# Kernel tuning notes

Hardware: AMD Instinct MI355X
Metric: run time of the kernel (lower is better)

Reference implementation:

```python
import jax, jax.numpy as jnp
import numpy as np

B, S, D, H, L, FF = 1, 2048, 512, 8, 4, 2048
DH = D // H


def _sincos(n, d):
    theta = 1.0 / (10000.0 ** (np.arange(0, d, 2, dtype=np.float64) / d))
    ang = np.arange(n, dtype=np.float64)[:, None] * theta[None, :]
    sin = np.repeat(np.sin(ang), 2, axis=-1).astype(np.float32)
    cos = np.repeat(np.cos(ang), 2, axis=-1).astype(np.float32)
    return jnp.asarray(sin), jnp.asarray(cos)  # [n, d]


def _rot(x):
    # rotate pairs: (x1, x2) -> (-x2, x1), interleaved
    x1, x2 = x[..., 0::2], x[..., 1::2]
    return jnp.stack([-x2, x1], axis=-1).reshape(x.shape)


def _theta_shift(x, sin, cos):
    return x * cos + _rot(x) * sin


def _decay_mask(n, h):
    # RetNet per-head decay gammas: 1 - exp(linspace(log(1/32), log(1/512), h))
    gammas = 1.0 - np.exp(np.linspace(np.log(1.0 / 32.0), np.log(1.0 / 512.0), h))
    dist = np.arange(n)[:, None] - np.arange(n)[None, :]
    m = np.where(dist >= 0, gammas[:, None, None] ** np.maximum(dist, 0), 0.0)
    return jnp.asarray(m, dtype=jnp.float32)  # [h, n, n]


def _ln(x, w, b, eps=1e-5):
    mu = x.mean(-1, keepdims=True)
    var = ((x - mu) ** 2).mean(-1, keepdims=True)
    return (x - mu) * jax.lax.rsqrt(var + eps) * w + b


def setup_inputs() -> dict:
    key = jax.random.key(0)
    ks = jax.random.split(key, 12)
    sc = 0.02
    nrm = lambda k, shp: jax.random.normal(k, shp, jnp.float32) * sc
    return {
        "x": jax.random.normal(ks[0], (B, S, D), jnp.float32),
        "pos_emb": nrm(ks[1], (5000, D)),
        "Wq": nrm(ks[2], (L, D, D)), "bq": jnp.zeros((L, D), jnp.float32),
        "Wk": nrm(ks[3], (L, D, D)), "bk": jnp.zeros((L, D), jnp.float32),
        "Wv": nrm(ks[4], (L, D, D)), "bv": jnp.zeros((L, D), jnp.float32),
        "Wg": nrm(ks[5], (L, D, D)), "bg": jnp.zeros((L, D), jnp.float32),
        "Wo": nrm(ks[6], (L, D, D)), "bo": jnp.zeros((L, D), jnp.float32),
        "ln1w": jnp.ones((L, D), jnp.float32), "ln1b": jnp.zeros((L, D), jnp.float32),
        "ln2w": jnp.ones((L, D), jnp.float32), "ln2b": jnp.zeros((L, D), jnp.float32),
        "W1": nrm(ks[7], (L, D, FF)), "b1": jnp.zeros((L, FF), jnp.float32),
        "W2": nrm(ks[8], (L, FF, D)), "b2": jnp.zeros((L, D), jnp.float32),
        "Wout": nrm(ks[9], (D, 1)), "bout": jnp.zeros((1,), jnp.float32),
    }


def reference(x, pos_emb, Wq, bq, Wk, bk, Wv, bv, Wg, bg, Wo, bo,
              ln1w, ln1b, ln2w, ln2b, W1, b1, W2, b2, Wout, bout):
    b, s, d = x.shape
    # faithful to source: pos_emb[:x.shape[0]] (requires B==1 to broadcast)
    x = x + pos_emb[: x.shape[0]]
    sin, cos = _sincos(s, DH)
    dmask = _decay_mask(s, H)  # [h, s, s]
    inv_scale = 1.0 / jnp.sqrt(jnp.float32(DH))

    def heads(t):  # [b,s,d] -> [b,h,s,dh]
        return t.reshape(b, s, H, DH).transpose(0, 2, 1, 3)

    for l in range(L):
        # --- multi-scale retention block (pre-LN) ---
        y = _ln(x, ln1w[l], ln1b[l])
        q = heads(y @ Wq[l] + bq[l])
        k = heads(y @ Wk[l] + bk[l])
        v = heads(y @ Wv[l] + bv[l])
        q = _theta_shift(q, sin, cos) * inv_scale
        k = _theta_shift(k, sin, cos)
        sim = jnp.einsum("bhnd,bhmd->bhnm", q, k) * dmask  # decay-masked QK^T
        ret = jnp.einsum("bhnm,bhmd->bhnd", sim, v)
        # per-head group norm (no affine)
        mu = ret.mean(-1, keepdims=True)
        var = ((ret - mu) ** 2).mean(-1, keepdims=True)
        ret = (ret - mu) * jax.lax.rsqrt(var + 1e-6)
        ret = ret.transpose(0, 2, 1, 3).reshape(b, s, d)
        g = jax.nn.silu(y @ Wg[l] + bg[l])
        x = x + (g * ret) @ Wo[l] + bo[l]
        # --- FFN block (pre-LN, swish) ---
        z = _ln(x, ln2w[l], ln2b[l])
        x = x + jax.nn.silu(z @ W1[l] + b1[l]) @ W2[l] + b2[l]

    return jax.nn.sigmoid(x @ Wout + bout)  # [b, s, 1]
```

## Files before the change

kernel.cpp:

```cpp
#include <hip/hip_runtime.h>
#include <math.h>
#include <stdint.h>

#define SEQ 2048
#define DMODEL 512
#define NH 8
#define DHEAD 64
#define NL 4
#define DFF 2048

typedef __attribute__((ext_vector_type(8))) short short8;
typedef __attribute__((ext_vector_type(4))) float f32x4;

__device__ __forceinline__ short f2bf(float f) {
  unsigned u = __float_as_uint(f);
  u += 0x7fffu + ((u >> 16) & 1u);
  return (short)(u >> 16);
}
__device__ __forceinline__ float silu_f(float x) { return x / (1.f + __expf(-x)); }

__device__ __forceinline__ void cp16(const void* g, void* l) {
  __builtin_amdgcn_global_load_lds(
      (const __attribute__((address_space(1))) unsigned*)(unsigned long long)(uintptr_t)g,
      (__attribute__((address_space(3))) unsigned*)(unsigned)(uintptr_t)l, 16, 0, 0);
}

struct TP { const float* src; short* dst; int rows, cols, base; };
struct TPs { TP t[7]; };
__global__ __launch_bounds__(256) void k_prep(TPs ts) {
  int bid = blockIdx.x;
  int di = 6;
  while (di > 0 && bid < ts.t[di].base) --di;
  TP d = ts.t[di];
  int local = bid - d.base;
  int tx = d.cols >> 5, ty = d.rows >> 5;
  int tpz = tx * ty;
  int z = local / tpz, rem = local - z * tpz;
  int bx = (rem % tx) * 32, by = (rem / tx) * 32;
  const float* src = d.src + (size_t)z * d.rows * d.cols;
  short* dst = d.dst + (size_t)z * d.rows * d.cols;
  __shared__ float tile[32][33];
  int txi = threadIdx.x & 31, tyi = threadIdx.x >> 5;
#pragma unroll
  for (int k = 0; k < 4; ++k)
    tile[tyi + k * 8][txi] = src[(size_t)(by + tyi + k * 8) * d.cols + bx + txi];
  __syncthreads();
#pragma unroll
  for (int k = 0; k < 4; ++k)
    dst[(size_t)(bx + tyi + k * 8) * d.rows + by + txi] = f2bf(tile[txi][tyi + k * 8]);
}

__global__ void k_init(const float* __restrict__ xi, const float* __restrict__ pos, float* __restrict__ xo,
                       float* __restrict__ sn, float* __restrict__ cs) {
  if (blockIdx.x < 1024) {
    int i = blockIdx.x * 256 + threadIdx.x;
    float4 a = ((const float4*)xi)[i];
    float4 p = ((const float4*)pos)[i & 127];
    a.x += p.x; a.y += p.y; a.z += p.z; a.w += p.w;
    ((float4*)xo)[i] = a;
  } else {
    int g = (blockIdx.x - 1024) * 256 + threadIdx.x;
    int s = g >> 5, p = g & 31;
    double inv = pow(10000.0, -(double)p / 32.0);
    double a = (double)s * inv;
    float sv = (float)sin(a), cv = (float)cos(a);
    sn[s * DHEAD + 2 * p] = sv; sn[s * DHEAD + 2 * p + 1] = sv;
    cs[s * DHEAD + 2 * p] = cv; cs[s * DHEAD + 2 * p + 1] = cv;
  }
}

__global__ __launch_bounds__(256) void k_ln(const float* __restrict__ x, const float* __restrict__ parts, int np,
                                            const float* __restrict__ w, const float* __restrict__ b,
                                            short* __restrict__ o, float eps, float* __restrict__ xout) {
  int wid = threadIdx.x >> 6, lane = threadIdx.x & 63;
  int row = blockIdx.x * 4 + wid;
  size_t base = (size_t)row * DMODEL + lane * 8;
  float4 v0 = *(const float4*)(x + base);
  float4 v1 = *(const float4*)(x + base + 4);
  for (int p = 0; p < np; ++p) {
    const float* pp = parts + (size_t)p * SEQ * DMODEL;
    float4 a0 = *(const float4*)(pp + base);
    float4 a1 = *(const float4*)(pp + base + 4);
    v0.x += a0.x; v0.y += a0.y; v0.z += a0.z; v0.w += a0.w;
    v1.x += a1.x; v1.y += a1.y; v1.z += a1.z; v1.w += a1.w;
  }
  if (xout) {
    *(float4*)(xout + base) = v0;
    *(float4*)(xout + base + 4) = v1;
  }
  float sm = v0.x + v0.y + v0.z + v0.w + v1.x + v1.y + v1.z + v1.w;
  float sq = v0.x * v0.x + v0.y * v0.y + v0.z * v0.z + v0.w * v0.w +
             v1.x * v1.x + v1.y * v1.y + v1.z * v1.z + v1.w * v1.w;
#pragma unroll
  for (int m = 1; m < 64; m <<= 1) { sm += __shfl_xor(sm, m); sq += __shfl_xor(sq, m); }
  float mu = sm * (1.f / 512.f);
  float rstd = rsqrtf(sq * (1.f / 512.f) - mu * mu + eps);
  const float* wr = w + lane * 8; const float* br = b + lane * 8;
  float vals[8] = {v0.x, v0.y, v0.z, v0.w, v1.x, v1.y, v1.z, v1.w};
  short t[8] __attribute__((aligned(16)));
#pragma unroll
  for (int i = 0; i < 8; ++i) t[i] = f2bf((vals[i] - mu) * rstd * wr[i] + br[i]);
  *(int4*)(o + (size_t)row * DMODEL + lane * 8) = *(int4*)t;
}

struct GB { const short* Bt; const float* bias; void* out; int mode; };
struct GP {
  const short* A;
  const float* sn; const float* cs;
  GB b[4];
  int M, N, K, kspl;
};

template <int BNT>
__global__ __launch_bounds__(256) void k_gemm(GP ga) {
  constexpr int NB = BNT / 32;
  constexpr int BRND = BNT / 32;
  const int z = blockIdx.z;
  GB gb; int k0, klen;
  if (ga.kspl > 0) { gb = ga.b[0]; k0 = z * ga.kspl; klen = ga.kspl; }
  else { gb = ga.b[z]; k0 = 0; klen = ga.K; }
  const int K = ga.K, N = ga.N, M = ga.M;
  const int n0 = blockIdx.x * BNT, m0 = blockIdx.y * 64;
  const int tid = threadIdx.x;
  const int w = tid >> 6, lane = tid & 63, l16 = lane & 15, quad = lane >> 4;
  const int wm = (w & 1) * 32, wn = (w >> 1) * (BNT / 2);
  const int nIter = klen >> 6;

  __shared__ __align__(16) short As[2][4096];
  __shared__ __align__(16) short Bs[2][BNT * 64];

  const short* Ab = ga.A + (size_t)m0 * K + k0;
  const short* Bb = gb.Bt + (size_t)n0 * K + k0;
  const int rsub = lane >> 3, cch = (lane & 7) ^ rsub;

  auto stage = [&](int buf, int it) {
#pragma unroll
    for (int c = 0; c < 2; ++c) {
      int seg = w + 4 * c;
      cp16(Ab + (size_t)(seg * 8 + rsub) * K + (it << 6) + cch * 8, &As[buf][seg * 512]);
    }
#pragma unroll
    for (int c = 0; c < BRND; ++c) {
      int seg = w + 4 * c;
      cp16(Bb + (size_t)(seg * 8 + rsub) * K + (it << 6) + cch * 8, &Bs[buf][seg * 512]);
    }
  };

  f32x4 acc[2][NB];
#pragma unroll
  for (int a = 0; a < 2; ++a)
#pragma unroll
    for (int b = 0; b < NB; ++b) acc[a][b] = {0.f, 0.f, 0.f, 0.f};

  stage(0, 0);
  for (int it = 0; it < nIter; ++it) {
    __syncthreads();
    if (it + 1 < nIter) stage((it + 1) & 1, it + 1);
    const short* as = As[it & 1];
    const short* bs = Bs[it & 1];
#pragma unroll
    for (int kki = 0; kki < 2; ++kki) {
      int ch = ((quad + 4 * kki) ^ (l16 & 7)) * 8;
      short8 af[2], bfv[NB];
#pragma unroll
      for (int a = 0; a < 2; ++a) af[a] = *(const short8*)&as[(wm + a * 16 + l16) * 64 + ch];
#pragma unroll
      for (int b = 0; b < NB; ++b) bfv[b] = *(const short8*)&bs[(wn + b * 16 + l16) * 64 + ch];
#pragma unroll
      for (int a = 0; a < 2; ++a)
#pragma unroll
        for (int b = 0; b < NB; ++b)
          acc[a][b] = __builtin_amdgcn_mfma_f32_16x16x32_bf16(af[a], bfv[b], acc[a][b], 0, 0, 0);
    }
  }

  const int mode = gb.mode;
#pragma unroll
  for (int a = 0; a < 2; ++a) {
#pragma unroll
    for (int b = 0; b < NB; ++b) {
      int row0 = m0 + wm + a * 16 + quad * 4;
      int col = n0 + wn + b * 16 + l16;
      float bi = (mode == 2 && z > 0) ? 0.f : gb.bias[col];
      float vals[4];
#pragma unroll
      for (int r = 0; r < 4; ++r) vals[r] = acc[a][b][r] + bi;
      if (mode == 5 || mode == 6) {
        float sc = (mode == 5) ? 0.125f : 1.f;
        int d = col & 63;
#pragma unroll
        for (int r = 0; r < 4; ++r) {
          int s = row0 + r;
          float vv = vals[r];
          float p = __shfl_xor(vv, 1);
          float rot = (col & 1) ? p : -p;
          float o = (vv * ga.cs[s * 64 + d] + rot * ga.sn[s * 64 + d]) * sc;
          ((short*)gb.out)[(size_t)s * DMODEL + col] = f2bf(o);
        }
      } else if (mode == 4) {
        short t4[4] __attribute__((aligned(8)));
#pragma unroll
        for (int r = 0; r < 4; ++r) t4[r] = f2bf(vals[r]);
        *(uint2*)&((short*)gb.out)[(size_t)col * M + row0] = *(const uint2*)t4;
      } else if (mode == 0) {
#pragma unroll
        for (int r = 0; r < 4; ++r) ((float*)gb.out)[(size_t)(row0 + r) * N + col] = vals[r];
      } else if (mode == 1) {
#pragma unroll
        for (int r = 0; r < 4; ++r) ((short*)gb.out)[(size_t)(row0 + r) * N + col] = f2bf(silu_f(vals[r]));
      } else {
        float* po = (float*)gb.out + (size_t)z * M * N;
#pragma unroll
        for (int r = 0; r < 4; ++r) po[(size_t)(row0 + r) * N + col] = vals[r];
      }
    }
  }
}

__global__ __launch_bounds__(256) void k_attn(const short* __restrict__ qb, const short* __restrict__ kb,
                                              const short* __restrict__ vtb, float* __restrict__ r0,
                                              float* __restrict__ r1) {
  int x = blockIdx.x, hd = blockIdx.y, jc = blockIdx.z;
  int ib = jc ? (31 - x) : x;
  int t = threadIdx.x;
  int w = t >> 6, lane = t & 63, l16 = lane & 15, quad = lane >> 4;
  __shared__ __align__(16) short smem[4 * 64 * 72];
  short* qs = smem;
  short* kt = smem + 4608;
  short* vt = smem + 9216;
  short* p  = smem + 13824;

  double stepd = (log(1.0 / 512.0) - log(1.0 / 32.0)) / 7.0;
  double gam = 1.0 - exp(log(1.0 / 32.0) + hd * stepd);
  float l2g = (float)(log(gam) * 1.4426950408889634);

  for (int c = t; c < 512; c += 256) {
    int r = c >> 3, d8 = (c & 7) * 8;
    *(short8*)&qs[r * 72 + d8] = *(const short8*)&qb[(size_t)(ib * 64 + r) * DMODEL + hd * DHEAD + d8];
  }
  f32x4 oacc[4];
#pragma unroll
  for (int b = 0; b < 4; ++b) oacc[b] = {0.f, 0.f, 0.f, 0.f};

  for (int jb = jc; jb <= ib; jb += 2) {
    __syncthreads();
    for (int c = t; c < 512; c += 256) {
      int r = c >> 3, d8 = (c & 7) * 8;
      *(short8*)&kt[r * 72 + d8] = *(const short8*)&kb[(size_t)(jb * 64 + r) * DMODEL + hd * DHEAD + d8];
      *(short8*)&vt[r * 72 + d8] = *(const short8*)&vtb[(size_t)(hd * DHEAD + r) * SEQ + jb * 64 + d8];
    }
    __syncthreads();
    f32x4 sacc[4];
#pragma unroll
    for (int b = 0; b < 4; ++b) sacc[b] = {0.f, 0.f, 0.f, 0.f};
#pragma unroll
    for (int kk = 0; kk < 64; kk += 32) {
      short8 af = *(const short8*)&qs[(w * 16 + l16) * 72 + kk + quad * 8];
#pragma unroll
      for (int b = 0; b < 4; ++b) {
        short8 bf_ = *(const short8*)&kt[(b * 16 + l16) * 72 + kk + quad * 8];
        sacc[b] = __builtin_amdgcn_mfma_f32_16x16x32_bf16(af, bf_, sacc[b], 0, 0, 0);
      }
    }
    int dtile = (ib - jb) * 64;
#pragma unroll
    for (int b = 0; b < 4; ++b) {
#pragma unroll
      for (int r = 0; r < 4; ++r) {
        int iloc = w * 16 + quad * 4 + r;
        int jloc = b * 16 + l16;
        int df = dtile + iloc - jloc;
        float dec = (df < 0) ? 0.f : exp2f(l2g * (float)df);
        p[iloc * 72 + jloc] = f2bf(sacc[b][r] * dec);
      }
    }
    __syncthreads();
#pragma unroll
    for (int kk = 0; kk < 64; kk += 32) {
      short8 af = *(const short8*)&vt[(w * 16 + l16) * 72 + kk + quad * 8];
#pragma unroll
      for (int b = 0; b < 4; ++b) {
        short8 bf_ = *(const short8*)&p[(b * 16 + l16) * 72 + kk + quad * 8];
        oacc[b] = __builtin_amdgcn_mfma_f32_16x16x32_bf16(af, bf_, oacc[b], 0, 0, 0);
      }
    }
  }
  __syncthreads();
  float* obuf = (float*)smem;
#pragma unroll
  for (int b = 0; b < 4; ++b) {
#pragma unroll
    for (int r = 0; r < 4; ++r) {
      int d = w * 16 + quad * 4 + r;
      int i = b * 16 + l16;
      obuf[i * 68 + d] = oacc[b][r];
    }
  }
  __syncthreads();
  float* rp = jc ? r1 : r0;
  for (int c = t; c < 1024; c += 256) {
    int r = c >> 4, d4 = (c & 15) * 4;
    *(float4*)&rp[(size_t)(ib * 64 + r) * DMODEL + hd * DHEAD + d4] = *(const float4*)&obuf[r * 68 + d4];
  }
}

__global__ __launch_bounds__(256) void k_retgate(const float* __restrict__ r0, const float* __restrict__ r1,
                                                 const float* __restrict__ g, short* __restrict__ o) {
  int wid = threadIdx.x >> 6, lane = threadIdx.x & 63;
  int row = blockIdx.x * 4 + wid;
  int s = row >> 3, hd = row & 7;
  size_t base = (size_t)s * DMODEL + hd * DHEAD + lane;
  float v = r0[base] + r1[base];
  float sm = v, sq = v * v;
#pragma unroll
  for (int m = 1; m < 64; m <<= 1) { sm += __shfl_xor(sm, m); sq += __shfl_xor(sq, m); }
  float mu = sm * (1.f / 64.f);
  float var = sq * (1.f / 64.f) - mu * mu;
  float rn = (v - mu) * rsqrtf(var + 1e-6f);
  o[base] = f2bf(silu_f(g[base]) * rn);
}

__global__ __launch_bounds__(256) void k_final(const float* __restrict__ x, const float* __restrict__ parts, int np,
                                               const float* __restrict__ w, const float* __restrict__ bo,
                                               float* __restrict__ o) {
  int wid = threadIdx.x >> 6, lane = threadIdx.x & 63;
  int row = blockIdx.x * 4 + wid;
  size_t base = (size_t)row * DMODEL + lane * 8;
  float4 a0 = *(const float4*)(x + base), a1 = *(const float4*)(x + base + 4);
  for (int p = 0; p < np; ++p) {
    const float* pp = parts + (size_t)p * SEQ * DMODEL;
    float4 b0 = *(const float4*)(pp + base);
    float4 b1 = *(const float4*)(pp + base + 4);
    a0.x += b0.x; a0.y += b0.y; a0.z += b0.z; a0.w += b0.w;
    a1.x += b1.x; a1.y += b1.y; a1.z += b1.z; a1.w += b1.w;
  }
  float4 w0 = *(const float4*)(w + lane * 8), w1 = *(const float4*)(w + lane * 8 + 4);
  float sm = a0.x * w0.x + a0.y * w0.y + a0.z * w0.z + a0.w * w0.w +
             a1.x * w1.x + a1.y * w1.y + a1.z * w1.z + a1.w * w1.w;
#pragma unroll
  for (int m = 1; m < 64; m <<= 1) sm += __shfl_xor(sm, m);
  if (lane == 0) o[row] = 1.f / (1.f + __expf(-(sm + bo[0])));
}

extern "C" void kernel_launch(void* const* d_in, const int* in_sizes, int n_in,
                              void* d_out, int out_size, void* d_ws, size_t ws_size,
                              hipStream_t stream) {
  const float* x_in = (const float*)d_in[0];
  const float* pos = (const float*)d_in[1];
  const float* Wq = (const float*)d_in[2];  const float* bq = (const float*)d_in[3];
  const float* Wk = (const float*)d_in[4];  const float* bk = (const float*)d_in[5];
  const float* Wv = (const float*)d_in[6];  const float* bv = (const float*)d_in[7];
  const float* Wg = (const float*)d_in[8];  const float* bg = (const float*)d_in[9];
  const float* Wo = (const float*)d_in[10]; const float* bo = (const float*)d_in[11];
  const float* ln1w = (const float*)d_in[12]; const float* ln1b = (const float*)d_in[13];
  const float* ln2w = (const float*)d_in[14]; const float* ln2b = (const float*)d_in[15];
  const float* W1 = (const float*)d_in[16]; const float* b1 = (const float*)d_in[17];
  const float* W2 = (const float*)d_in[18]; const float* b2 = (const float*)d_in[19];
  const float* Wout = (const float*)d_in[20]; const float* bout = (const float*)d_in[21];
  float* out = (float*)d_out;

  char* ws = (char*)d_ws;
  size_t off = 0;
  auto alloc = [&](size_t bytes) -> void* {
    void* p = ws + off;
    off += (bytes + 255) & ~(size_t)255;
    return p;
  };
  const size_t DD = (size_t)DMODEL * DMODEL;
  const size_t SD = (size_t)SEQ * DMODEL;
  short* wqt = (short*)alloc((size_t)NL * DD * 2);
  short* wkt = (short*)alloc((size_t)NL * DD * 2);
  short* wvt = (short*)alloc((size_t)NL * DD * 2);
  short* wgt = (short*)alloc((size_t)NL * DD * 2);
  short* wot = (short*)alloc((size_t)NL * DD * 2);
  short* w1t = (short*)alloc((size_t)NL * DMODEL * DFF * 2);
  short* w2t = (short*)alloc((size_t)NL * DMODEL * DFF * 2);
  float* xb = (float*)alloc(SD * 4);
  short* ybf = (short*)alloc(SD * 2);
  float* graw = (float*)alloc(SD * 4);
  short* qb = (short*)alloc(SD * 2);
  short* kb = (short*)alloc(SD * 2);
  short* vtb = (short*)alloc(SD * 2);
  float* ret0 = (float*)alloc(SD * 4);
  float* ret1 = (float*)alloc(SD * 4);
  short* grb = (short*)alloc(SD * 2);
  short* zbf = (short*)alloc(SD * 2);
  short* hbf = (short*)alloc((size_t)SEQ * DFF * 2);
  float* sint = (float*)alloc((size_t)SEQ * DHEAD * 4);
  float* cost = (float*)alloc((size_t)SEQ * DHEAD * 4);
  float* wpart = (float*)alloc(2 * SD * 4);
  float* fpart = (float*)alloc(4 * SD * 4);

  TPs tp;
  tp.t[0] = TP{Wq, wqt, DMODEL, DMODEL, 0};
  tp.t[1] = TP{Wk, wkt, DMODEL, DMODEL, 1024};
  tp.t[2] = TP{Wv, wvt, DMODEL, DMODEL, 2048};
  tp.t[3] = TP{Wg, wgt, DMODEL, DMODEL, 3072};
  tp.t[4] = TP{Wo, wot, DMODEL, DMODEL, 4096};
  tp.t[5] = TP{W1, w1t, DMODEL, DFF, 5120};
  tp.t[6] = TP{W2, w2t, DFF, DMODEL, 9216};
  k_prep<<<13312, 256, 0, stream>>>(tp);
  k_init<<<1280, 256, 0, stream>>>(x_in, pos, xb, sint, cost);

  for (int l = 0; l < NL; ++l) {
    k_ln<<<SEQ / 4, 256, 0, stream>>>(xb, fpart, l == 0 ? 0 : 4,
                                      ln1w + l * DMODEL, ln1b + l * DMODEL, ybf, 1e-5f,
                                      l == 0 ? nullptr : xb);

    GP gq{};
    gq.A = ybf; gq.sn = sint; gq.cs = cost;
    gq.b[0] = GB{wqt + l * DD, bq + l * DMODEL, qb, 5};
    gq.b[1] = GB{wkt + l * DD, bk + l * DMODEL, kb, 6};
    gq.b[2] = GB{wvt + l * DD, bv + l * DMODEL, vtb, 4};
    gq.b[3] = GB{wgt + l * DD, bg + l * DMODEL, graw, 0};
    gq.M = SEQ; gq.N = DMODEL; gq.K = DMODEL; gq.kspl = 0;
    k_gemm<64><<<dim3(DMODEL / 64, SEQ / 64, 4), 256, 0, stream>>>(gq);

    k_attn<<<dim3(32, NH, 2), 256, 0, stream>>>(qb, kb, vtb, ret0, ret1);
    k_retgate<<<SEQ * NH / 4, 256, 0, stream>>>(ret0, ret1, graw, grb);

    GP gw{};
    gw.A = grb;
    gw.b[0] = GB{wot + l * DD, bo + l * DMODEL, wpart, 2};
    gw.M = SEQ; gw.N = DMODEL; gw.K = DMODEL; gw.kspl = 256;
    k_gemm<64><<<dim3(DMODEL / 64, SEQ / 64, 2), 256, 0, stream>>>(gw);

    k_ln<<<SEQ / 4, 256, 0, stream>>>(xb, wpart, 2,
                                      ln2w + l * DMODEL, ln2b + l * DMODEL, zbf, 1e-5f, xb);

    GP g1{};
    g1.A = zbf;
    g1.b[0] = GB{w1t + (size_t)l * DMODEL * DFF, b1 + l * DFF, hbf, 1};
    g1.M = SEQ; g1.N = DFF; g1.K = DMODEL; g1.kspl = 0;
    k_gemm<64><<<dim3(DFF / 64, SEQ / 64, 1), 256, 0, stream>>>(g1);

    GP g2{};
    g2.A = hbf;
    g2.b[0] = GB{w2t + (size_t)l * DMODEL * DFF, b2 + l * DMODEL, fpart, 2};
    g2.M = SEQ; g2.N = DMODEL; g2.K = DFF; g2.kspl = 512;
    k_gemm<64><<<dim3(DMODEL / 64, SEQ / 64, 4), 256, 0, stream>>>(g2);
  }
  k_final<<<SEQ / 4, 256, 0, stream>>>(xb, fpart, 4, Wout, bout, out);
}
```

Before: 521.0 us.

## Enlarge GEMM tiles to 128 rows and fuse QKVG weights into one wide GEMM

The QKVG projection weights are packed into one contiguous [4*512, 512] transposed buffer per layer. A single wide GEMM now covers all four, picking each output's epilogue by column block instead of by grid z. The GEMM kernel tile grows from 64 to 128 rows, and to 128 columns for the QKVG and FFN1 GEMMs, to raise data reuse per block and cut loads from global memory. The trade-off is fewer blocks per launch and more registers per thread, which may leave CUs underused.

```diff
diff --git a/kernel.cpp b/kernel.cpp
--- a/kernel.cpp
+++ b/kernel.cpp
@@ -25,7 +25,7 @@
       (__attribute__((address_space(3))) unsigned*)(unsigned)(uintptr_t)l, 16, 0, 0);
 }
 
-struct TP { const float* src; short* dst; int rows, cols, base; };
+struct TP { const float* src; short* dst; int rows, cols, base, lstride; };
 struct TPs { TP t[7]; };
 __global__ __launch_bounds__(256) void k_prep(TPs ts) {
   int bid = blockIdx.x;
@@ -38,7 +38,7 @@
   int z = local / tpz, rem = local - z * tpz;
   int bx = (rem % tx) * 32, by = (rem / tx) * 32;
   const float* src = d.src + (size_t)z * d.rows * d.cols;
-  short* dst = d.dst + (size_t)z * d.rows * d.cols;
+  short* dst = d.dst + (size_t)z * d.lstride;
   __shared__ float tile[32][33];
   int txi = threadIdx.x & 31, tyi = threadIdx.x >> 5;
 #pragma unroll
@@ -108,26 +108,28 @@
   const short* A;
   const float* sn; const float* cs;
   GB b[4];
-  int M, N, K, kspl;
+  int M, N, K, kspl, wide;
 };
 
-template <int BNT>
+template <int BN>
 __global__ __launch_bounds__(256) void k_gemm(GP ga) {
-  constexpr int NB = BNT / 32;
-  constexpr int BRND = BNT / 32;
+  constexpr int NBW = BN / 32;
+  constexpr int ARND = 4;
+  constexpr int BRND = BN / 32;
   const int z = blockIdx.z;
   GB gb; int k0, klen;
   if (ga.kspl > 0) { gb = ga.b[0]; k0 = z * ga.kspl; klen = ga.kspl; }
-  else { gb = ga.b[z]; k0 = 0; klen = ga.K; }
+  else { gb = ga.b[0]; k0 = 0; klen = ga.K; }
   const int K = ga.K, N = ga.N, M = ga.M;
-  const int n0 = blockIdx.x * BNT, m0 = blockIdx.y * 64;
+  const int n0 = blockIdx.x * BN, m0 = blockIdx.y * 128;
+  if (ga.wide) gb = ga.b[n0 >> 9];
   const int tid = threadIdx.x;
   const int w = tid >> 6, lane = tid & 63, l16 = lane & 15, quad = lane >> 4;
-  const int wm = (w & 1) * 32, wn = (w >> 1) * (BNT / 2);
+  const int wm = (w & 1) * 64, wn = (w >> 1) * (BN / 2);
   const int nIter = klen >> 6;
 
-  __shared__ __align__(16) short As[2][4096];
-  __shared__ __align__(16) short Bs[2][BNT * 64];
+  __shared__ __align__(16) short As[2][8192];
+  __shared__ __align__(16) short Bs[2][BN * 64];
 
   const short* Ab = ga.A + (size_t)m0 * K + k0;
   const short* Bb = gb.Bt + (size_t)n0 * K + k0;
@@ -135,7 +137,7 @@
 
   auto stage = [&](int buf, int it) {
 #pragma unroll
-    for (int c = 0; c < 2; ++c) {
+    for (int c = 0; c < ARND; ++c) {
       int seg = w + 4 * c;
       cp16(Ab + (size_t)(seg * 8 + rsub) * K + (it << 6) + cch * 8, &As[buf][seg * 512]);
     }
@@ -146,11 +148,11 @@
     }
   };
 
-  f32x4 acc[2][NB];
-#pragma unroll
-  for (int a = 0; a < 2; ++a)
-#pragma unroll
-    for (int b = 0; b < NB; ++b) acc[a][b] = {0.f, 0.f, 0.f, 0.f};
+  f32x4 acc[4][NBW];
+#pragma unroll
+  for (int a = 0; a < 4; ++a)
+#pragma unroll
+    for (int b = 0; b < NBW; ++b) acc[a][b] = {0.f, 0.f, 0.f, 0.f};
 
   stage(0, 0);
   for (int it = 0; it < nIter; ++it) {
@@ -161,57 +163,58 @@
 #pragma unroll
     for (int kki = 0; kki < 2; ++kki) {
       int ch = ((quad + 4 * kki) ^ (l16 & 7)) * 8;
-      short8 af[2], bfv[NB];
-#pragma unroll
-      for (int a = 0; a < 2; ++a) af[a] = *(const short8*)&as[(wm + a * 16 + l16) * 64 + ch];
-#pragma unroll
-      for (int b = 0; b < NB; ++b) bfv[b] = *(const short8*)&bs[(wn + b * 16 + l16) * 64 + ch];
-#pragma unroll
-      for (int a = 0; a < 2; ++a)
-#pragma unroll
-        for (int b = 0; b < NB; ++b)
+      short8 af[4], bfv[NBW];
+#pragma unroll
+      for (int a = 0; a < 4; ++a) af[a] = *(const short8*)&as[(wm + a * 16 + l16) * 64 + ch];
+#pragma unroll
+      for (int b = 0; b < NBW; ++b) bfv[b] = *(const short8*)&bs[(wn + b * 16 + l16) * 64 + ch];
+#pragma unroll
+      for (int a = 0; a < 4; ++a)
+#pragma unroll
+        for (int b = 0; b < NBW; ++b)
           acc[a][b] = __builtin_amdgcn_mfma_f32_16x16x32_bf16(af[a], bfv[b], acc[a][b], 0, 0, 0);
     }
   }
 
   const int mode = gb.mode;
 #pragma unroll
-  for (int a = 0; a < 2; ++a) {
-#pragma unroll
-    for (int b = 0; b < NB; ++b) {
+  for (int a = 0; a < 4; ++a) {
+#pragma unroll
+    for (int b = 0; b < NBW; ++b) {
       int row0 = m0 + wm + a * 16 + quad * 4;
       int col = n0 + wn + b * 16 + l16;
-      float bi = (mode == 2 && z > 0) ? 0.f : gb.bias[col];
+      int colO = ga.wide ? (col & 511) : col;
+      float bi = (mode == 2 && z > 0) ? 0.f : gb.bias[colO];
       float vals[4];
 #pragma unroll
       for (int r = 0; r < 4; ++r) vals[r] = acc[a][b][r] + bi;
       if (mode == 5 || mode == 6) {
         float sc = (mode == 5) ? 0.125f : 1.f;
-        int d = col & 63;
+        int d = colO & 63;
 #pragma unroll
         for (int r = 0; r < 4; ++r) {
           int s = row0 + r;
           float vv = vals[r];
           float p = __shfl_xor(vv, 1);
-          float rot = (col & 1) ? p : -p;
+          float rot = (colO & 1) ? p : -p;
           float o = (vv * ga.cs[s * 64 + d] + rot * ga.sn[s * 64 + d]) * sc;
-          ((short*)gb.out)[(size_t)s * DMODEL + col] = f2bf(o);
+          ((short*)gb.out)[(size_t)s * DMODEL + colO] = f2bf(o);
         }
       } else if (mode == 4) {
         short t4[4] __attribute__((aligned(8)));
 #pragma unroll
         for (int r = 0; r < 4; ++r) t4[r] = f2bf(vals[r]);
-        *(uint2*)&((short*)gb.out)[(size_t)col * M + row0] = *(const uint2*)t4;
+        *(uint2*)&((short*)gb.out)[(size_t)colO * M + row0] = *(const uint2*)t4;
       } else if (mode == 0) {
 #pragma unroll
-        for (int r = 0; r < 4; ++r) ((float*)gb.out)[(size_t)(row0 + r) * N + col] = vals[r];
+        for (int r = 0; r < 4; ++r) ((float*)gb.out)[(size_t)(row0 + r) * DMODEL + colO] = vals[r];
       } else if (mode == 1) {
 #pragma unroll
         for (int r = 0; r < 4; ++r) ((short*)gb.out)[(size_t)(row0 + r) * N + col] = f2bf(silu_f(vals[r]));
       } else {
-        float* po = (float*)gb.out + (size_t)z * M * N;
-#pragma unroll
-        for (int r = 0; r < 4; ++r) po[(size_t)(row0 + r) * N + col] = vals[r];
+        float* po = (float*)gb.out + (size_t)z * M * DMODEL;
+#pragma unroll
+        for (int r = 0; r < 4; ++r) po[(size_t)(row0 + r) * DMODEL + colO] = vals[r];
       }
     }
   }
@@ -368,10 +371,7 @@
   };
   const size_t DD = (size_t)DMODEL * DMODEL;
   const size_t SD = (size_t)SEQ * DMODEL;
-  short* wqt = (short*)alloc((size_t)NL * DD * 2);
-  short* wkt = (short*)alloc((size_t)NL * DD * 2);
-  short* wvt = (short*)alloc((size_t)NL * DD * 2);
-  short* wgt = (short*)alloc((size_t)NL * DD * 2);
+  short* wqkvg = (short*)alloc((size_t)NL * 4 * DD * 2);
   short* wot = (short*)alloc((size_t)NL * DD * 2);
   short* w1t = (short*)alloc((size_t)NL * DMODEL * DFF * 2);
   short* w2t = (short*)alloc((size_t)NL * DMODEL * DFF * 2);
@@ -392,13 +392,13 @@
   float* fpart = (float*)alloc(4 * SD * 4);
 
   TPs tp;
-  tp.t[0] = TP{Wq, wqt, DMODEL, DMODEL, 0};
-  tp.t[1] = TP{Wk, wkt, DMODEL, DMODEL, 1024};
-  tp.t[2] = TP{Wv, wvt, DMODEL, DMODEL, 2048};
-  tp.t[3] = TP{Wg, wgt, DMODEL, DMODEL, 3072};
-  tp.t[4] = TP{Wo, wot, DMODEL, DMODEL, 4096};
-  tp.t[5] = TP{W1, w1t, DMODEL, DFF, 5120};
-  tp.t[6] = TP{W2, w2t, DFF, DMODEL, 9216};
+  tp.t[0] = TP{Wq, wqkvg + 0 * DD, DMODEL, DMODEL, 0, (int)(4 * DD)};
+  tp.t[1] = TP{Wk, wqkvg + 1 * DD, DMODEL, DMODEL, 1024, (int)(4 * DD)};
+  tp.t[2] = TP{Wv, wqkvg + 2 * DD, DMODEL, DMODEL, 2048, (int)(4 * DD)};
+  tp.t[3] = TP{Wg, wqkvg + 3 * DD, DMODEL, DMODEL, 3072, (int)(4 * DD)};
+  tp.t[4] = TP{Wo, wot, DMODEL, DMODEL, 4096, (int)DD};
+  tp.t[5] = TP{W1, w1t, DMODEL, DFF, 5120, DMODEL * DFF};
+  tp.t[6] = TP{W2, w2t, DFF, DMODEL, 9216, DMODEL * DFF};
   k_prep<<<13312, 256, 0, stream>>>(tp);
   k_init<<<1280, 256, 0, stream>>>(x_in, pos, xb, sint, cost);
 
@@ -409,12 +409,12 @@
 
     GP gq{};
     gq.A = ybf; gq.sn = sint; gq.cs = cost;
-    gq.b[0] = GB{wqt + l * DD, bq + l * DMODEL, qb, 5};
-    gq.b[1] = GB{wkt + l * DD, bk + l * DMODEL, kb, 6};
-    gq.b[2] = GB{wvt + l * DD, bv + l * DMODEL, vtb, 4};
-    gq.b[3] = GB{wgt + l * DD, bg + l * DMODEL, graw, 0};
-    gq.M = SEQ; gq.N = DMODEL; gq.K = DMODEL; gq.kspl = 0;
-    k_gemm<64><<<dim3(DMODEL / 64, SEQ / 64, 4), 256, 0, stream>>>(gq);
+    gq.b[0] = GB{wqkvg + (size_t)l * 4 * DD, bq + l * DMODEL, qb, 5};
+    gq.b[1] = GB{wqkvg + (size_t)l * 4 * DD, bk + l * DMODEL, kb, 6};
+    gq.b[2] = GB{wqkvg + (size_t)l * 4 * DD, bv + l * DMODEL, vtb, 4};
+    gq.b[3] = GB{wqkvg + (size_t)l * 4 * DD, bg + l * DMODEL, graw, 0};
+    gq.M = SEQ; gq.N = 4 * DMODEL; gq.K = DMODEL; gq.kspl = 0; gq.wide = 1;
+    k_gemm<128><<<dim3(16, SEQ / 128, 1), 256, 0, stream>>>(gq);
 
     k_attn<<<dim3(32, NH, 2), 256, 0, stream>>>(qb, kb, vtb, ret0, ret1);
     k_retgate<<<SEQ * NH / 4, 256, 0, stream>>>(ret0, ret1, graw, grb);
@@ -422,8 +422,8 @@
     GP gw{};
     gw.A = grb;
     gw.b[0] = GB{wot + l * DD, bo + l * DMODEL, wpart, 2};
-    gw.M = SEQ; gw.N = DMODEL; gw.K = DMODEL; gw.kspl = 256;
-    k_gemm<64><<<dim3(DMODEL / 64, SEQ / 64, 2), 256, 0, stream>>>(gw);
+    gw.M = SEQ; gw.N = DMODEL; gw.K = DMODEL; gw.kspl = 256; gw.wide = 0;
+    k_gemm<64><<<dim3(DMODEL / 64, SEQ / 128, 2), 256, 0, stream>>>(gw);
 
     k_ln<<<SEQ / 4, 256, 0, stream>>>(xb, wpart, 2,
                                       ln2w + l * DMODEL, ln2b + l * DMODEL, zbf, 1e-5f, xb);
@@ -431,14 +431,14 @@
     GP g1{};
     g1.A = zbf;
     g1.b[0] = GB{w1t + (size_t)l * DMODEL * DFF, b1 + l * DFF, hbf, 1};
-    g1.M = SEQ; g1.N = DFF; g1.K = DMODEL; g1.kspl = 0;
-    k_gemm<64><<<dim3(DFF / 64, SEQ / 64, 1), 256, 0, stream>>>(g1);
+    g1.M = SEQ; g1.N = DFF; g1.K = DMODEL; g1.kspl = 0; g1.wide = 0;
+    k_gemm<128><<<dim3(DFF / 128, SEQ / 128, 1), 256, 0, stream>>>(g1);
 
     GP g2{};
     g2.A = hbf;
     g2.b[0] = GB{w2t + (size_t)l * DMODEL * DFF, b2 + l * DMODEL, fpart, 2};
-    g2.M = SEQ; g2.N = DMODEL; g2.K = DFF; g2.kspl = 512;
-    k_gemm<64><<<dim3(DMODEL / 64, SEQ / 64, 4), 256, 0, stream>>>(g2);
+    g2.M = SEQ; g2.N = DMODEL; g2.K = DFF; g2.kspl = 512; g2.wide = 0;
+    k_gemm<64><<<dim3(DMODEL / 64, SEQ / 128, 4), 256, 0, stream>>>(g2);
   }
   k_final<<<SEQ / 4, 256, 0, stream>>>(xb, fpart, 4, Wout, bout, out);
 }
```

New measurement: 570.5 us. 1.09x slower.
